# Kernel tuning notes

Hardware: AMD Instinct MI355X
Metric: run time of the kernel (lower is better)

## Reference

```python
import jax, jax.numpy as jnp
import numpy as np

O, C_IN, P, D = 256, 256, 96, 2
KH, KW = 51, 51


def setup_inputs() -> dict:
    key = jax.random.key(0)
    k1, k2, k3 = jax.random.split(key, 3)
    # coordinate grid in [-1, 1], shape (1, D, KH, KW) like a normalized meshgrid
    ys = jnp.linspace(-1.0, 1.0, KH, dtype=jnp.float32)
    xs = jnp.linspace(-1.0, 1.0, KW, dtype=jnp.float32)
    gy, gx = jnp.meshgrid(ys, xs, indexing="ij")
    x = jnp.stack([gy, gx], axis=0)[None]  # (1, 2, KH, KW)
    # learned point coordinates, trunc-normal-ish in [-1, 1]
    weight_coord = jnp.clip(0.3 * jax.random.normal(k1, (O, P, D), dtype=jnp.float32), -1.0, 1.0)
    # per-point radius, initialized to init_radius
    radius = jnp.full((O, P, 1, 1), 0.5, dtype=jnp.float32)
    # point weights
    weights = 0.02 * jax.random.normal(k2, (O, C_IN, P), dtype=jnp.float32)
    return {"x": x, "weight_coord": weight_coord, "radius": radius, "weights": weights}


def reference(x, weight_coord, radius, weights):
    o, p, d = weight_coord.shape
    spatial = x.shape[2:]  # (KH, KW)
    n = int(np.prod(spatial))
    coords = x.reshape(d, n).T  # (N, D)
    # broadcast coord diff + L1 distance over dim_linear: (O, P, N)
    dist = jnp.sum(jnp.abs(weight_coord[:, :, None, :] - coords[None, None, :, :]), axis=-1)
    # triangular basis
    vals = jax.nn.relu(1.0 - dist / radius.reshape(o, p, 1))  # (O, P, N)
    # count of points covering each location, used to normalize
    count = jnp.sum(vals != 0, axis=1, keepdims=True)  # (O, 1, N), int
    weighted = vals / (count.astype(vals.dtype) + 1e-6)
    # batched small matmul over points: (O, C_in, P) @ (O, P, N) -> (O, C_in, N)
    kernels = jnp.einsum("ocp,opn->ocn", weights, weighted)
    kernels = kernels.reshape(o, weights.shape[1], *spatial)
    # dim_linear == 2 branch: transpose last two dims, flip along dim 2
    kernels = jnp.flip(jnp.swapaxes(kernels, -2, -1), axis=2)
    return kernels
```

## Files before the change

### kernel.cpp

```cpp
#include <hip/hip_runtime.h>

#define O_DIM 256
#define C_DIM 256
#define P_DIM 96
#define KHW 51
#define NSP 2601
#define NST 41
#define CSPLIT 4
#define CB 64
#define PITCH 68

typedef __attribute__((ext_vector_type(8))) short short8v;
typedef __attribute__((ext_vector_type(4))) float float4v;
typedef __attribute__((ext_vector_type(4), aligned(16))) float float4a;
typedef __attribute__((ext_vector_type(4), aligned(4))) float float4u;

static __device__ __forceinline__ unsigned f2bf(float f) {
  union { float f; unsigned u; } v; v.f = f;
  return (v.u + 0x7FFFu + ((v.u >> 16) & 1u)) >> 16;
}
static __device__ __forceinline__ unsigned cvtpk(float lo, float hi) {
  unsigned r;
  asm("v_cvt_pk_bf16_f32 %0, %1, %2" : "=v"(r) : "v"(lo), "v"(hi));
  return r;
}

__global__ __launch_bounds__(256, 4) void smp_fused(
    const float* __restrict__ xg,
    const float* __restrict__ wc,
    const float* __restrict__ rad,
    const float* __restrict__ wts,
    float* __restrict__ out)
{
  __shared__ float Ylds[56];
  __shared__ float pyL[96], pxL[96], prL[96];
  __shared__ __align__(16) float Sl[2][64 * PITCH];

  const int b = blockIdx.x;
  const int o = b >> 2;
  const int cq = b & 3;
  const int tid = threadIdx.x;
  const int wave = tid >> 6;
  const int lane = tid & 63;
  const int row16 = lane & 15;
  const int kgrp = lane >> 4;

  if (tid < 51) Ylds[tid] = xg[tid * KHW];
  if (tid < 96) {
    pyL[tid] = wc[((size_t)o * P_DIM + tid) * 2];
    pxL[tid] = wc[((size_t)o * P_DIM + tid) * 2 + 1];
    prL[tid] = 1.0f / rad[(size_t)o * P_DIM + tid];
  }

  short8v wfr[4][3];
  {
    const float* Wo = wts + ((size_t)o * C_DIM + cq * CB) * P_DIM;
#pragma unroll
    for (int mf = 0; mf < 4; ++mf) {
      const float* src = Wo + (mf * 16 + row16) * P_DIM;
#pragma unroll
      for (int ks = 0; ks < 3; ++ks) {
        const float4 a4 = *(const float4*)(src + ks * 32 + kgrp * 8);
        const float4 c4 = *(const float4*)(src + ks * 32 + kgrp * 8 + 4);
        short8v f;
        f[0] = (short)f2bf(a4.x); f[1] = (short)f2bf(a4.y);
        f[2] = (short)f2bf(a4.z); f[3] = (short)f2bf(a4.w);
        f[4] = (short)f2bf(c4.x); f[5] = (short)f2bf(c4.y);
        f[6] = (short)f2bf(c4.z); f[7] = (short)f2bf(c4.w);
        wfr[mf][ks] = f;
      }
    }
  }
  __syncthreads();

  const int jb = wave * 16 + row16;
  const int q = tid & 15;
  const int h = tid >> 4;
  const size_t obase = ((size_t)o * C_DIM + cq * CB) * NSP;

  for (int st = 0; st < NST; ++st) {
    const int jl = st * 64 + jb;
    const int jc = jl < NSP ? jl : NSP - 1;
    const int i = jc / KHW;
    const int jj = jc - i * KHW;
    const float gy = Ylds[jj];
    const float gx = Ylds[50 - i];

    float4v acc[4];
#pragma unroll
    for (int mf = 0; mf < 4; ++mf) acc[mf] = (float4v){0.f, 0.f, 0.f, 0.f};

    int cnt = 0;
#pragma unroll
    for (int ks = 0; ks < 3; ++ks) {
      const int pb = ks * 32 + kgrp * 8;
      const float4a py0 = *(const float4a*)&pyL[pb];
      const float4a py1 = *(const float4a*)&pyL[pb + 4];
      const float4a px0 = *(const float4a*)&pxL[pb];
      const float4a px1 = *(const float4a*)&pxL[pb + 4];
      const float4a pr0 = *(const float4a*)&prL[pb];
      const float4a pr1 = *(const float4a*)&prL[pb + 4];
      float s[8], v[8];
#pragma unroll
      for (int j = 0; j < 4; ++j) {
        s[j]     = fmaf(fabsf(py0[j] - gy) + fabsf(px0[j] - gx), -pr0[j], 1.0f);
        s[j + 4] = fmaf(fabsf(py1[j] - gy) + fabsf(px1[j] - gx), -pr1[j], 1.0f);
      }
#pragma unroll
      for (int j = 0; j < 8; ++j) {
        v[j] = s[j] > 0.0f ? s[j] : 0.0f;
        cnt += (s[j] > 0.0f);
      }
      union { unsigned u[4]; short8v sv; } bfr;
#pragma unroll
      for (int jp = 0; jp < 4; ++jp) bfr.u[jp] = cvtpk(v[2 * jp], v[2 * jp + 1]);
#pragma unroll
      for (int mf = 0; mf < 4; ++mf)
        acc[mf] = __builtin_amdgcn_mfma_f32_16x16x32_bf16(
            wfr[mf][ks], bfr.sv, acc[mf], 0, 0, 0);
    }
    cnt += __shfl_xor(cnt, 16);
    cnt += __shfl_xor(cnt, 32);
    const float inv = __builtin_amdgcn_rcpf((float)cnt + 1e-6f);

    float* sl = &Sl[st & 1][0];
#pragma unroll
    for (int mf = 0; mf < 4; ++mf)
#pragma unroll
      for (int r = 0; r < 4; ++r)
        sl[(mf * 16 + kgrp * 4 + r) * PITCH + jb] = acc[mf][r] * inv;

    __syncthreads();

    if (st < NST - 1) {
#pragma unroll
      for (int i2 = 0; i2 < 4; ++i2) {
        const int row = h * 4 + i2;
        const float4a vv = *(const float4a*)&sl[row * PITCH + q * 4];
        float4u sv = {vv[0], vv[1], vv[2], vv[3]};
        *(float4u*)(out + obase + (size_t)row * NSP + st * 64 + q * 4) = sv;
      }
    } else {
      const int rem = NSP - (NST - 1) * 64;
#pragma unroll
      for (int i2 = 0; i2 < 4; ++i2) {
        const int row = h * 4 + i2;
        const float4a vv = *(const float4a*)&sl[row * PITCH + q * 4];
        float* gp = out + obase + (size_t)row * NSP + st * 64 + q * 4;
        if (q * 4 + 3 < rem) {
          float4u sv = {vv[0], vv[1], vv[2], vv[3]};
          *(float4u*)gp = sv;
        } else if (q * 4 < rem) {
#pragma unroll
          for (int r2 = 0; r2 < 4; ++r2)
            if (q * 4 + r2 < rem) gp[r2] = vv[r2];
        }
      }
    }
  }
}

extern "C" void kernel_launch(void* const* d_in, const int* in_sizes, int n_in,
                              void* d_out, int out_size, void* d_ws, size_t ws_size,
                              hipStream_t stream) {
  const float* xg  = (const float*)d_in[0];
  const float* wcp = (const float*)d_in[1];
  const float* rad = (const float*)d_in[2];
  const float* wts = (const float*)d_in[3];
  float* out = (float*)d_out;
  hipLaunchKernelGGL(smp_fused, dim3(O_DIM * CSPLIT), dim3(256), 0, stream,
                     xg, wcp, rad, wts, out);
}
```

Before: 234.5 us.

## Restructure work split to 16-channel groups with bf16 LDS staging

Each block now handles 16 output channels instead of 64, with 1024 threads and 16 waves. Every wave computes 16 spatial columns per round using a single MFMA per k-step. All results are staged in LDS as bf16 across the whole spatial range, and after one barrier each wave streams one contiguous output row. This removes the 41 per-tile barriers and makes the global stores row-contiguous. In exchange the basis evaluation is recomputed four times more often, the output is rounded to bf16 precision, and the large LDS footprint likely leaves one block per CU, so compute and store phases are serialized.

Measured after the change: 384.1 us. 63.8% more time.

```diff
diff --git a/kernel.cpp b/kernel.cpp
--- a/kernel.cpp
+++ b/kernel.cpp
@@ -5,10 +5,8 @@
 #define P_DIM 96
 #define KHW 51
 #define NSP 2601
-#define NST 41
-#define CSPLIT 4
-#define CB 64
-#define PITCH 68
+#define NR 11
+#define PR 2608
 
 typedef __attribute__((ext_vector_type(8))) short short8v;
 typedef __attribute__((ext_vector_type(4))) float float4v;
@@ -24,21 +22,24 @@
   asm("v_cvt_pk_bf16_f32 %0, %1, %2" : "=v"(r) : "v"(lo), "v"(hi));
   return r;
 }
+static __device__ __forceinline__ float bcast(unsigned u) {
+  union { unsigned u; float f; } v; v.u = u; return v.f;
+}
 
-__global__ __launch_bounds__(256, 4) void smp_fused(
+__global__ __launch_bounds__(1024, 1) void smp_fused(
     const float* __restrict__ xg,
     const float* __restrict__ wc,
     const float* __restrict__ rad,
     const float* __restrict__ wts,
     float* __restrict__ out)
 {
-  __shared__ float Ylds[56];
-  __shared__ float pyL[96], pxL[96], prL[96];
-  __shared__ __align__(16) float Sl[2][64 * PITCH];
+  __shared__ float Ylds[52];
+  __shared__ __align__(16) float pyL[96], pxL[96], prL[96];
+  __shared__ __align__(16) unsigned short RBuf[16 * PR];
 
   const int b = blockIdx.x;
-  const int o = b >> 2;
-  const int cq = b & 3;
+  const int o = b >> 4;
+  const int cg = b & 15;
   const int tid = threadIdx.x;
   const int wave = tid >> 6;
   const int lane = tid & 63;
@@ -52,44 +53,32 @@
     prL[tid] = 1.0f / rad[(size_t)o * P_DIM + tid];
   }
 
-  short8v wfr[4][3];
+  short8v wfr[3];
   {
-    const float* Wo = wts + ((size_t)o * C_DIM + cq * CB) * P_DIM;
+    const float* src = wts + ((size_t)o * C_DIM + cg * 16 + row16) * P_DIM;
 #pragma unroll
-    for (int mf = 0; mf < 4; ++mf) {
-      const float* src = Wo + (mf * 16 + row16) * P_DIM;
-#pragma unroll
-      for (int ks = 0; ks < 3; ++ks) {
-        const float4 a4 = *(const float4*)(src + ks * 32 + kgrp * 8);
-        const float4 c4 = *(const float4*)(src + ks * 32 + kgrp * 8 + 4);
-        short8v f;
-        f[0] = (short)f2bf(a4.x); f[1] = (short)f2bf(a4.y);
-        f[2] = (short)f2bf(a4.z); f[3] = (short)f2bf(a4.w);
-        f[4] = (short)f2bf(c4.x); f[5] = (short)f2bf(c4.y);
-        f[6] = (short)f2bf(c4.z); f[7] = (short)f2bf(c4.w);
-        wfr[mf][ks] = f;
-      }
+    for (int ks = 0; ks < 3; ++ks) {
+      const float4 a4 = *(const float4*)(src + ks * 32 + kgrp * 8);
+      const float4 c4 = *(const float4*)(src + ks * 32 + kgrp * 8 + 4);
+      short8v f;
+      f[0] = (short)f2bf(a4.x); f[1] = (short)f2bf(a4.y);
+      f[2] = (short)f2bf(a4.z); f[3] = (short)f2bf(a4.w);
+      f[4] = (short)f2bf(c4.x); f[5] = (short)f2bf(c4.y);
+      f[6] = (short)f2bf(c4.z); f[7] = (short)f2bf(c4.w);
+      wfr[ks] = f;
     }
   }
   __syncthreads();
 
-  const int jb = wave * 16 + row16;
-  const int q = tid & 15;
-  const int h = tid >> 4;
-  const size_t obase = ((size_t)o * C_DIM + cq * CB) * NSP;
-
-  for (int st = 0; st < NST; ++st) {
-    const int jl = st * 64 + jb;
-    const int jc = jl < NSP ? jl : NSP - 1;
+  for (int r = 0; r < NR; ++r) {
+    const int jlc = r * 256 + wave * 16 + row16;
+    const int jc = jlc < NSP ? jlc : NSP - 1;
     const int i = jc / KHW;
     const int jj = jc - i * KHW;
     const float gy = Ylds[jj];
     const float gx = Ylds[50 - i];
 
-    float4v acc[4];
-#pragma unroll
-    for (int mf = 0; mf < 4; ++mf) acc[mf] = (float4v){0.f, 0.f, 0.f, 0.f};
-
+    float4v acc = (float4v){0.f, 0.f, 0.f, 0.f};
     int cnt = 0;
 #pragma unroll
     for (int ks = 0; ks < 3; ++ks) {
@@ -114,48 +103,41 @@
       union { unsigned u[4]; short8v sv; } bfr;
 #pragma unroll
       for (int jp = 0; jp < 4; ++jp) bfr.u[jp] = cvtpk(v[2 * jp], v[2 * jp + 1]);
-#pragma unroll
-      for (int mf = 0; mf < 4; ++mf)
-        acc[mf] = __builtin_amdgcn_mfma_f32_16x16x32_bf16(
-            wfr[mf][ks], bfr.sv, acc[mf], 0, 0, 0);
+      acc = __builtin_amdgcn_mfma_f32_16x16x32_bf16(wfr[ks], bfr.sv, acc, 0, 0, 0);
     }
     cnt += __shfl_xor(cnt, 16);
     cnt += __shfl_xor(cnt, 32);
     const float inv = __builtin_amdgcn_rcpf((float)cnt + 1e-6f);
 
-    float* sl = &Sl[st & 1][0];
+    if (jlc < NSP) {
 #pragma unroll
-    for (int mf = 0; mf < 4; ++mf)
+      for (int r2 = 0; r2 < 4; ++r2)
+        RBuf[(kgrp * 4 + r2) * PR + jlc] = (unsigned short)f2bf(acc[r2] * inv);
+    }
+  }
+  __syncthreads();
+
+  {
+    const unsigned short* rb = &RBuf[wave * PR];
+    float* gp = out + ((size_t)o * C_DIM + cg * 16 + wave) * NSP;
 #pragma unroll
-      for (int r = 0; r < 4; ++r)
-        sl[(mf * 16 + kgrp * 4 + r) * PITCH + jb] = acc[mf][r] * inv;
-
-    __syncthreads();
-
-    if (st < NST - 1) {
+    for (int it = 0; it < 10; ++it) {
+      const int j = it * 256 + lane * 4;
+      const uint2 u = *(const uint2*)&rb[j];
+      float4u v = {bcast(u.x << 16), bcast(u.x & 0xFFFF0000u),
+                   bcast(u.y << 16), bcast(u.y & 0xFFFF0000u)};
+      *(float4u*)(gp + j) = v;
+    }
+    const int j = 2560 + lane * 4;
+    if (j + 4 <= NSP) {
+      const uint2 u = *(const uint2*)&rb[j];
+      float4u v = {bcast(u.x << 16), bcast(u.x & 0xFFFF0000u),
+                   bcast(u.y << 16), bcast(u.y & 0xFFFF0000u)};
+      *(float4u*)(gp + j) = v;
+    } else if (j < NSP) {
 #pragma unroll
-      for (int i2 = 0; i2 < 4; ++i2) {
-        const int row = h * 4 + i2;
-        const float4a vv = *(const float4a*)&sl[row * PITCH + q * 4];
-        float4u sv = {vv[0], vv[1], vv[2], vv[3]};
-        *(float4u*)(out + obase + (size_t)row * NSP + st * 64 + q * 4) = sv;
-      }
-    } else {
-      const int rem = NSP - (NST - 1) * 64;
-#pragma unroll
-      for (int i2 = 0; i2 < 4; ++i2) {
-        const int row = h * 4 + i2;
-        const float4a vv = *(const float4a*)&sl[row * PITCH + q * 4];
-        float* gp = out + obase + (size_t)row * NSP + st * 64 + q * 4;
-        if (q * 4 + 3 < rem) {
-          float4u sv = {vv[0], vv[1], vv[2], vv[3]};
-          *(float4u*)gp = sv;
-        } else if (q * 4 < rem) {
-#pragma unroll
-          for (int r2 = 0; r2 < 4; ++r2)
-            if (q * 4 + r2 < rem) gp[r2] = vv[r2];
-        }
-      }
+      for (int r2 = 0; r2 < 4; ++r2)
+        if (j + r2 < NSP) gp[j + r2] = bcast(((unsigned)rb[j + r2]) << 16);
     }
   }
 }
@@ -168,6 +150,6 @@
   const float* rad = (const float*)d_in[2];
   const float* wts = (const float*)d_in[3];
   float* out = (float*)d_out;
-  hipLaunchKernelGGL(smp_fused, dim3(O_DIM * CSPLIT), dim3(256), 0, stream,
+  hipLaunchKernelGGL(smp_fused, dim3(O_DIM * 16), dim3(1024), 0, stream,
                      xg, wcp, rad, wts, out);
 }
```
